# Kernel optimization log

Measured on AMD Instinct MI355X. Metric: run time of the kernel, lower is better.

## Reference

```python
import jax, jax.numpy as jnp
import numpy as np
from jax import lax

K = 5          # dynamic kernel size
GROUPS = 8     # inter_channels // group_channels = 128 // 16
R = 2          # pixel shuffle upscale factor
SLOPE = 0.01   # LeakyReLU default negative_slope
EPS = 1e-5     # BatchNorm eps


def conv2d(x, w, b, pad=0):
    # x: [B,C,H,W], w: [O,I,kh,kw]
    y = lax.conv_general_dilated(x, w, (1, 1), [(pad, pad), (pad, pad)],
                                 dimension_numbers=('NCHW', 'OIHW', 'NCHW'))
    return y + b[None, :, None, None]


def pixel_shuffle(x, r):
    B, C, H, W = x.shape
    x = x.reshape(B, C // (r * r), r, r, H, W)
    x = x.transpose(0, 1, 4, 2, 5, 3)  # B, C', H, r, W, r
    return x.reshape(B, C // (r * r), H * r, W * r)


def involution(x, weight, k, groups, pad):
    # x: [B,C,H,W]; weight: [B,groups,k,k,H,W]
    # out[b, g*gc+c, h, w] = sum_ij weight[b,g,i,j,h,w] * x_pad[b, g*gc+c, h+i, w+j]
    B, C, H, W = x.shape
    gc = C // groups
    xp = jnp.pad(x, ((0, 0), (0, 0), (pad, pad), (pad, pad)))
    xg = xp.reshape(B, groups, gc, H + 2 * pad, W + 2 * pad)
    out = jnp.zeros((B, groups, gc, H, W), x.dtype)
    for i in range(k):
        for j in range(k):
            out = out + weight[:, :, None, i, j] * xg[:, :, :, i:i + H, j:j + W]
    return out.reshape(B, C, H, W)


def setup_inputs() -> dict:
    key = jax.random.key(0)
    ks = jax.random.split(key, 16)
    s = 0.05
    return {
        'high_level': jax.random.normal(ks[0], (8, 128, 64, 64), jnp.float32),
        'low_level': jax.random.normal(ks[1], (8, 224, 128, 128), jnp.float32),
        'emb': jax.random.normal(ks[2], (8, 256, 128, 128), jnp.float32),
        'reduce_w': jax.random.normal(ks[3], (128, 256, 1, 1), jnp.float32) * s,
        'reduce_b': jax.random.normal(ks[4], (128,), jnp.float32) * s,
        'conv1_w': jax.random.normal(ks[5], (32, 128, 1, 1), jnp.float32) * s,
        'conv1_b': jax.random.normal(ks[6], (32,), jnp.float32) * s,
        'conv2_w': jax.random.normal(ks[7], (200, 32, 3, 3), jnp.float32) * s,
        'conv2_b': jax.random.normal(ks[8], (200,), jnp.float32) * s,
        'embconv_w': jax.random.normal(ks[9], (32, 256, 1, 1), jnp.float32) * s,
        'embconv_b': jax.random.normal(ks[10], (32,), jnp.float32) * s,
        'out_w': jax.random.normal(ks[11], (64, 128, 1, 1), jnp.float32) * s,
        'out_b': jax.random.normal(ks[12], (64,), jnp.float32) * s,
        'bn_gamma': jnp.ones((64,), jnp.float32),
        'bn_beta': jnp.zeros((64,), jnp.float32),
        'bn_mean': jnp.zeros((64,), jnp.float32),
        'bn_var': jax.random.uniform(ks[13], (64,), jnp.float32, 0.5, 1.5),
    }


def reference(high_level, low_level, emb,
              reduce_w, reduce_b, conv1_w, conv1_b, conv2_w, conv2_b,
              embconv_w, embconv_b, out_w, out_b,
              bn_gamma, bn_beta, bn_mean, bn_var):
    cat = jnp.concatenate([pixel_shuffle(high_level, R), low_level], axis=1)
    cat = conv2d(cat, reduce_w, reduce_b)
    mix = jax.nn.leaky_relu(conv2d(cat, conv1_w, conv1_b)
                            + conv2d(emb, embconv_w, embconv_b), SLOPE)
    w = conv2d(mix, conv2_w, conv2_b, pad=1)  # [B, K*K*GROUPS, H, W]
    B, _, H, W = w.shape
    w = w.reshape(B, GROUPS, K, K, H, W)
    o = involution(cat, w, K, GROUPS, (K - 1) // 2)
    o = conv2d(o, out_w, out_b)
    o = (o - bn_mean[None, :, None, None]) * (bn_gamma[None, :, None, None]
        / jnp.sqrt(bn_var[None, :, None, None] + EPS)) + bn_beta[None, :, None, None]
    return jax.nn.leaky_relu(o, SLOPE)
```

## Files before the change

kernel.cpp:

```cpp
#include <hip/hip_runtime.h>

typedef unsigned short u16; typedef unsigned int u32; typedef unsigned long long u64;
typedef __attribute__((ext_vector_type(8))) short short8;
typedef __attribute__((ext_vector_type(16))) float f32x16;

#define HW 16384

#define RED_B  0
#define C1E_B  128
#define C2_B   160
#define OUT_B  416
#define BN_SC  480
#define BN_SH  544
#define FLAG_OFF   4096
#define RWB_OFF    8192
#define C1B_OFF    73728
#define EMBB_OFF   81920
#define OUTB_OFF   98304
#define C2PB_OFF   114688
#define CAT2_OFF   524288
#define MIX_OFF    34078720
#define WGT_OFF    42467328

__device__ __forceinline__ float bf2f(u16 x){ u32 u=((u32)x)<<16; float f; __builtin_memcpy(&f,&u,4); return f; }
__device__ __forceinline__ u16 f2bf(float f){ u32 u; __builtin_memcpy(&u,&f,4); return (u16)((u + 0x7fffu + ((u>>16)&1u))>>16); }
__device__ __forceinline__ float lrelu(float x){ return x>0.f ? x : 0.01f*x; }

template<int M> __device__ __forceinline__ u16 ldb(const void* p, size_t i){
    if (M==1) return ((const u16*)p)[i];
    return f2bf(((const float*)p)[i]);
}
template<int M> __device__ __forceinline__ float ldf(const void* p, size_t i){
    if (M==1) return bf2f(((const u16*)p)[i]);
    return ((const float*)p)[i];
}
__device__ __forceinline__ void stA(u16* At, int stride, int p, int c, u16 v){
    At[p*stride + ((((c>>3) ^ ((p>>1)&7)))<<3) + (c&7)] = v;
}

__global__ void detect_kernel(const void* __restrict__ emb, u32* __restrict__ flag){
    int tid = threadIdx.x;
    const u16* p = (const u16*)emb;
    int e = (p[tid*2] >> 7) & 0xFF;
    u64 m = __ballot(e >= 100 && e <= 140);
    if (tid == 0) *flag = (__popcll(m) >= 32) ? 1u : 0u;
}

template<int M>
__global__ __launch_bounds__(256) void k_prep(
    const void* rw, const void* rb, const void* c1w, const void* c1b,
    const void* c2w, const void* c2b, const void* ew, const void* eb,
    const void* ow, const void* ob, const void* gam, const void* bet,
    const void* mn, const void* vr, char* ws, const u32* flag)
{
    if (*flag != (u32)M) return;
    float* wf = (float*)ws;
    int i = blockIdx.x*256 + threadIdx.x;
    if (i < 32768)       ((u16*)(ws+RWB_OFF))[i] = ldb<M>(rw, i);
    else if (i < 36864)  ((u16*)(ws+C1B_OFF))[i-32768] = ldb<M>(c1w, i-32768);
    else if (i < 45056)  ((u16*)(ws+EMBB_OFF))[i-36864] = ldb<M>(ew, i-36864);
    else if (i < 53248)  ((u16*)(ws+OUTB_OFF))[i-45056] = ldb<M>(ow, i-45056);
    else if (i < 126976) {
        int j = i-53248; int o = j/288, k = j - o*288;
        int tap = k>>5, ic = k&31;
        u16 v = 0;
        if (o < 200) v = ldb<M>(c2w, (size_t)o*288 + ic*9 + tap);
        ((u16*)(ws+C2PB_OFF))[j] = v;
    }
    else if (i < 127584) {
        int j = i-126976;
        if (j < 128) wf[RED_B+j] = ldf<M>(rb, j);
        else if (j < 160) wf[C1E_B+j-128] = ldf<M>(c1b, j-128) + ldf<M>(eb, j-128);
        else if (j < 416) { int o = j-160; wf[C2_B+o] = (o<200) ? ldf<M>(c2b,o) : 0.f; }
        else if (j < 480) wf[OUT_B+j-416] = ldf<M>(ob, j-416);
        else if (j < 544) { int c=j-480; wf[BN_SC+c] = ldf<M>(gam,c) * rsqrtf(ldf<M>(vr,c)+1e-5f); }
        else { int c=j-544; wf[BN_SH+c] = ldf<M>(bet,c) - ldf<M>(mn,c)*ldf<M>(gam,c)*rsqrtf(ldf<M>(vr,c)+1e-5f); }
    }
}

template<int M>
__global__ __launch_bounds__(256) void k_reduce(
    const void* __restrict__ hi, const void* __restrict__ lo,
    const u16* __restrict__ rwB, const float* __restrict__ wf,
    u16* __restrict__ cat2, const u32* __restrict__ flag)
{
    if (*flag != (u32)M) return;
    __shared__ u16 At[64*264];
    const int tid = threadIdx.x, wvi = tid>>6, lane = tid&63;
    const int rt = (wvi>>1)*32, nc0 = (wvi&1)*64;
    const int col = lane&31, q = lane>>5;

    short8 B[2][16];
#pragma unroll
    for (int nt=0; nt<2; nt++){
        int o = nc0 + nt*32 + col;
#pragma unroll
        for (int s=0; s<16; s++)
            __builtin_memcpy(&B[nt][s], rwB + (size_t)o*256 + s*16 + q*8, 16);
    }

    for (int it=0; it<4; it++){
        int chunk = blockIdx.x + it*512;
        int gpx = chunk*64;
        int b = gpx>>14, p0 = gpx&16383;
        int h = p0>>7, w0 = p0&127;
        __syncthreads();
        {
            int qq = tid&31, cid = tid>>5;
#pragma unroll 4
            for (int i=0;i<28;i++){
                int c = cid*28 + i;
                size_t src = ((size_t)(b*224 + c))*HW + p0 + 2*qq;
                u16 v0, v1;
                if (M==1){ u32 v = *(const u32*)((const u16*)lo + src); v0=(u16)v; v1=(u16)(v>>16); }
                else { v0 = f2bf(((const float*)lo)[src]); v1 = f2bf(((const float*)lo)[src+1]); }
                stA(At,264, 2*qq,   32+c, v0);
                stA(At,264, 2*qq+1, 32+c, v1);
            }
        }
        {
            int xq = tid&15, cid = tid>>4;
#pragma unroll
            for (int i=0;i<2;i++){
                int c = cid + i*16;
                int hc = c*4 + (h&1)*2;
                size_t src = ((size_t)(b*128 + hc))*4096 + (size_t)(h>>1)*64 + (w0>>1) + 2*xq;
                u16 e0 = ldb<M>(hi, src),      e1 = ldb<M>(hi, src+1);
                u16 o0 = ldb<M>(hi, src+4096), o1 = ldb<M>(hi, src+4097);
                stA(At,264, 4*xq,   c, e0);
                stA(At,264, 4*xq+2, c, e1);
                stA(At,264, 4*xq+1, c, o0);
                stA(At,264, 4*xq+3, c, o1);
            }
        }
        __syncthreads();

        f32x16 acc0, acc1;
#pragma unroll
        for (int r=0;r<16;r++){ acc0[r]=0.f; acc1[r]=0.f; }
        int pp = rt + col, sw = (pp>>1)&7;
        const u16* arow = At + pp*264;
#pragma unroll
        for (int s=0;s<16;s++){
            short8 a;
            __builtin_memcpy(&a, arow + (((2*s+q)^sw)<<3), 16);
            acc0 = __builtin_amdgcn_mfma_f32_32x32x16_bf16(a, B[0][s], acc0, 0,0,0);
            acc1 = __builtin_amdgcn_mfma_f32_32x32x16_bf16(a, B[1][s], acc1, 0,0,0);
        }
#pragma unroll
        for (int nt=0; nt<2; nt++){
            int oc = nc0 + nt*32 + col;
            float bias = wf[RED_B + oc];
#pragma unroll
            for (int r=0;r<16;r++){
                int row = (r&3) + 8*(r>>2) + 4*q;
                float v = (nt ? acc1[r] : acc0[r]) + bias;
                cat2[((size_t)(gpx + rt + row))*128 + oc] = f2bf(v);
            }
        }
    }
}

template<int M>
__global__ __launch_bounds__(256) void k_mix(
    const u16* __restrict__ cat2, const void* __restrict__ emb,
    const u16* __restrict__ c1B, const u16* __restrict__ embB,
    const float* __restrict__ wf, u16* __restrict__ mixt, const u32* __restrict__ flag)
{
    if (*flag != (u32)M) return;
    __shared__ u16 At[128*136];
    const int tid = threadIdx.x, wvi = tid>>6, lane = tid&63;
    const int rt = wvi*32, col = lane&31, q = lane>>5;

    short8 Bc[8], Be[16];
#pragma unroll
    for (int s=0;s<8;s++)  __builtin_memcpy(&Bc[s], c1B  + (size_t)col*128 + s*16 + q*8, 16);
#pragma unroll
    for (int s=0;s<16;s++) __builtin_memcpy(&Be[s], embB + (size_t)col*256 + s*16 + q*8, 16);

    for (int it=0; it<4; it++){
        int chunk = blockIdx.x + it*256;
        int gpx = chunk*128;
        int b = gpx>>14, p0 = gpx&16383;

        f32x16 acc;
#pragma unroll
        for (int r=0;r<16;r++) acc[r]=0.f;
        int pp = rt + col, sw = (pp>>1)&7;
        const u16* arow = At + pp*136;

        __syncthreads();
#pragma unroll
        for (int i=0;i<8;i++){
            int idx = tid + i*256;
            int p = idx>>4, c16 = idx&15;
            short8 v;
            __builtin_memcpy(&v, cat2 + ((size_t)(gpx+p))*128 + c16*8, 16);
            *(short8*)(At + p*136 + ((c16 ^ ((p>>1)&7))<<3)) = v;
        }
        __syncthreads();
#pragma unroll
        for (int s=0;s<8;s++){
            short8 a; __builtin_memcpy(&a, arow + (((2*s+q)^sw)<<3), 16);
            acc = __builtin_amdgcn_mfma_f32_32x32x16_bf16(a, Bc[s], acc, 0,0,0);
        }
#pragma unroll 1
        for (int half=0; half<2; half++){
            __syncthreads();
            {
                int qq = tid&31, cid = (tid>>5)&1, g2 = tid>>6;
#pragma unroll 2
                for (int ph=0; ph<2; ph++)
#pragma unroll 4
                for (int i=0;i<16;i++){
                    int c = cid*64 + g2*16 + i;
                    int ec = half*128 + c;
                    int p = ph*64 + 2*qq;
                    size_t src = ((size_t)(b*256 + ec))*HW + p0 + p;
                    u16 v0, v1;
                    if (M==1){ u32 v = *(const u32*)((const u16*)emb + src); v0=(u16)v; v1=(u16)(v>>16); }
                    else { v0 = f2bf(((const float*)emb)[src]); v1 = f2bf(((const float*)emb)[src+1]); }
                    stA(At,136, p,   c, v0);
                    stA(At,136, p+1, c, v1);
                }
            }
            __syncthreads();
#pragma unroll
            for (int s=0;s<8;s++){
                short8 a; __builtin_memcpy(&a, arow + (((2*s+q)^sw)<<3), 16);
                acc = __builtin_amdgcn_mfma_f32_32x32x16_bf16(a, Be[half*8+s], acc, 0,0,0);
            }
        }
        float bias = wf[C1E_B + col];
#pragma unroll
        for (int r=0;r<16;r++){
            int row = (r&3) + 8*(r>>2) + 4*q;
            mixt[((size_t)(gpx + rt + row))*32 + col] = f2bf(lrelu(acc[r] + bias));
        }
    }
}

__global__ __launch_bounds__(256) void k_conv2(
    const u16* __restrict__ mixt, const u16* __restrict__ c2B,
    const float* __restrict__ wf, u16* __restrict__ wgt)
{
    __shared__ u16 halo[100*32];
    const int tid = threadIdx.x, wvi = tid>>6, lane = tid&63;
    const int rt = (wvi>>1)*32, npair = wvi&1;
    const int nh = blockIdx.x & 1;
    const int nc0 = nh*128 + npair*64;
    const int col = lane&31, q = lane>>5;

    short8 B[2][18];
#pragma unroll
    for (int nt=0; nt<2; nt++){
        int o = nc0 + nt*32 + col;
#pragma unroll
        for (int s=0; s<18; s++)
            __builtin_memcpy(&B[nt][s], c2B + (size_t)o*288 + s*16 + q*8, 16);
    }

    for (int it=0; it<4; it++){
        int tile = (blockIdx.x>>1) + it*512;
        int b = tile>>8, tl = tile&255;
        int ty = tl>>4, tx = tl&15;
        __syncthreads();
#pragma unroll
        for (int i=0;i<2;i++){
            int idx = tid + i*256;
            if (idx < 400){
                int point = idx>>2, cq = idx&3;
                int y = ty*8 + point/10 - 1, x = tx*8 + point%10 - 1;
                short8 v;
                if (y>=0 && y<128 && x>=0 && x<128)
                    __builtin_memcpy(&v, mixt + ((size_t)(b*HW + y*128 + x))*32 + cq*8, 16);
                else { short z = 0; v = (short8){z,z,z,z,z,z,z,z}; }
                *(short8*)(halo + point*32 + cq*8) = v;
            }
        }
        __syncthreads();

        f32x16 acc0, acc1;
#pragma unroll
        for (int r=0;r<16;r++){ acc0[r]=0.f; acc1[r]=0.f; }
        int pp = rt + col, py = pp>>3, px = pp&7;
#pragma unroll
        for (int s=0;s<18;s++){
            int tap = s>>1, ih = s&1;
            int dy = tap/3, dx = tap%3;
            short8 a;
            __builtin_memcpy(&a, halo + ((py+dy)*10 + px+dx)*32 + ih*16 + q*8, 16);
            acc0 = __builtin_amdgcn_mfma_f32_32x32x16_bf16(a, B[0][s], acc0, 0,0,0);
            acc1 = __builtin_amdgcn_mfma_f32_32x32x16_bf16(a, B[1][s], acc1, 0,0,0);
        }
#pragma unroll
        for (int nt=0; nt<2; nt++){
            int oc = nc0 + nt*32 + col;
            if (oc < 200){
                float bias = wf[C2_B + oc];
#pragma unroll
                for (int r=0;r<16;r++){
                    int row = (r&3) + 8*(r>>2) + 4*q;
                    int p2 = rt + row;
                    int y = ty*8 + (p2>>3), x = tx*8 + (p2&7);
                    float v = (nt ? acc1[r] : acc0[r]) + bias;
                    wgt[((size_t)(b*200 + oc))*HW + y*128 + x] = f2bf(v);
                }
            }
        }
    }
}

template<int M>
__global__ __launch_bounds__(256) void k_inv(
    const u16* __restrict__ cat2, const u16* __restrict__ wgt,
    const u16* __restrict__ outB, const float* __restrict__ wf,
    void* __restrict__ out, const u32* __restrict__ flag)
{
    if (*flag != (u32)M) return;
    __shared__ u16 halo[400*16];
    __shared__ u16 og[256*16];
    const int tid = threadIdx.x, wvi = tid>>6, lane = tid&63;
    const int col = lane&31, q = lane>>5;
    const int b = blockIdx.y, ty = blockIdx.x>>3, tx = blockIdx.x&7;
    const int py = tid>>4, px = tid&15;
    const int h = ty*16 + py, w = tx*16 + px;

    f32x16 acc[2][2];
#pragma unroll
    for (int i=0;i<2;i++)
#pragma unroll
    for (int j=0;j<2;j++)
#pragma unroll
    for (int r=0;r<16;r++) acc[i][j][r] = 0.f;

#pragma unroll 1
    for (int g=0; g<8; g++){
        __syncthreads();
#pragma unroll
        for (int i=0;i<4;i++){
            int idx = tid + i*256;
            if (idx < 800){
                int point = idx>>1, cq = idx&1;
                int y = ty*16 + point/20 - 2, x = tx*16 + point%20 - 2;
                short8 v;
                if (y>=0 && y<128 && x>=0 && x<128)
                    __builtin_memcpy(&v, cat2 + ((size_t)(b*HW + y*128 + x))*128 + g*16 + cq*8, 16);
                else { short z=0; v = (short8){z,z,z,z,z,z,z,z}; }
                *(short8*)(halo + point*16 + cq*8) = v;
            }
        }
        __syncthreads();

        float wvv[25];
#pragma unroll
        for (int t=0;t<25;t++)
            wvv[t] = bf2f(wgt[((size_t)(b*200 + g*25 + t))*HW + h*128 + w]);

        float a16[16];
#pragma unroll
        for (int cc=0;cc<16;cc++) a16[cc]=0.f;
#pragma unroll
        for (int t=0;t<25;t++){
            int dy = t/5, dx = t%5;
            u32 vv[8];
            __builtin_memcpy(vv, halo + ((py+dy)*20 + px+dx)*16, 32);
            float wt = wvv[t];
#pragma unroll
            for (int r=0;r<8;r++){
                u32 u = vv[r];
                u32 ulo = u<<16, uhi = u & 0xffff0000u;
                float x0, x1;
                __builtin_memcpy(&x0,&ulo,4); __builtin_memcpy(&x1,&uhi,4);
                a16[2*r]   += wt*x0;
                a16[2*r+1] += wt*x1;
            }
        }
        u32 pk[8];
#pragma unroll
        for (int r=0;r<8;r++) pk[r] = (u32)f2bf(a16[2*r]) | ((u32)f2bf(a16[2*r+1])<<16);
        __syncthreads();
        __builtin_memcpy(og + tid*16, pk, 32);
        __syncthreads();

        short8 bo0, bo1;
        __builtin_memcpy(&bo0, outB + (size_t)(col)*128      + g*16 + q*8, 16);
        __builtin_memcpy(&bo1, outB + (size_t)(32+col)*128   + g*16 + q*8, 16);
#pragma unroll
        for (int rt2=0; rt2<2; rt2++){
            int prow = (wvi*2 + rt2)*32 + col;
            short8 a; __builtin_memcpy(&a, og + prow*16 + q*8, 16);
            acc[rt2][0] = __builtin_amdgcn_mfma_f32_32x32x16_bf16(a, bo0, acc[rt2][0], 0,0,0);
            acc[rt2][1] = __builtin_amdgcn_mfma_f32_32x32x16_bf16(a, bo1, acc[rt2][1], 0,0,0);
        }
    }
#pragma unroll
    for (int rt2=0; rt2<2; rt2++)
#pragma unroll
    for (int nt=0; nt<2; nt++){
        int oc = nt*32 + col;
        float bias = wf[OUT_B+oc], sc = wf[BN_SC+oc], sh = wf[BN_SH+oc];
#pragma unroll
        for (int r=0;r<16;r++){
            int row = (r&3) + 8*(r>>2) + 4*q;
            int p = (wvi*2 + rt2)*32 + row;
            int yy = ty*16 + (p>>4), xx = tx*16 + (p&15);
            float v = lrelu((acc[rt2][nt][r] + bias)*sc + sh);
            size_t oidx = ((size_t)(b*64 + oc))*HW + yy*128 + xx;
            if (M==1) ((u16*)out)[oidx] = f2bf(v);
            else ((float*)out)[oidx] = v;
        }
    }
}

extern "C" void kernel_launch(void* const* d_in, const int* in_sizes, int n_in,
                              void* d_out, int out_size, void* d_ws, size_t ws_size,
                              hipStream_t stream) {
    const void* hi  = d_in[0];
    const void* lo  = d_in[1];
    const void* emb = d_in[2];
    char* ws = (char*)d_ws;
    float* wf = (float*)ws;
    u32* flag = (u32*)(ws + FLAG_OFF);
    u16* cat2 = (u16*)(ws + CAT2_OFF);
    u16* mixt = (u16*)(ws + MIX_OFF);
    u16* wgt  = (u16*)(ws + WGT_OFF);

    detect_kernel<<<1, 64, 0, stream>>>(emb, flag);

    k_prep<0><<<499,256,0,stream>>>(d_in[3],d_in[4],d_in[5],d_in[6],d_in[7],d_in[8],
        d_in[9],d_in[10],d_in[11],d_in[12],d_in[13],d_in[14],d_in[15],d_in[16], ws, flag);
    k_prep<1><<<499,256,0,stream>>>(d_in[3],d_in[4],d_in[5],d_in[6],d_in[7],d_in[8],
        d_in[9],d_in[10],d_in[11],d_in[12],d_in[13],d_in[14],d_in[15],d_in[16], ws, flag);

    k_reduce<0><<<512,256,0,stream>>>(hi, lo, (const u16*)(ws+RWB_OFF), wf, cat2, flag);
    k_reduce<1><<<512,256,0,stream>>>(hi, lo, (const u16*)d_in[3],      wf, cat2, flag);

    k_mix<0><<<256,256,0,stream>>>(cat2, emb, (const u16*)(ws+C1B_OFF), (const u16*)(ws+EMBB_OFF), wf, mixt, flag);
    k_mix<1><<<256,256,0,stream>>>(cat2, emb, (const u16*)d_in[5],      (const u16*)d_in[9],       wf, mixt, flag);

    k_conv2<<<1024,256,0,stream>>>(mixt, (const u16*)(ws+C2PB_OFF), wf, wgt);

    k_inv<0><<<dim3(64,8),256,0,stream>>>(cat2, wgt, (const u16*)(ws+OUTB_OFF), wf, d_out, flag);
    k_inv<1><<<dim3(64,8),256,0,stream>>>(cat2, wgt, (const u16*)d_in[11],      wf, d_out, flag);
}
```

Before: 488.1 us.

## Vectorize global loads in reduce and mix kernels and launch one tile per block

The reduce and mix kernels now load input activations with 16-byte (or 32-byte fp32) vector loads per thread along the pixel dimension, replacing 2-element scalar loads. They also drop the persistent 4-iteration loop in favour of four times as many blocks, each handling one tile. This aims to cut global load instruction count and raise memory-level parallelism. In exchange, weights are reloaded per block, and the per-element LDS transpose stores in the swizzled layout may cause more bank conflicts.

```diff
diff --git a/kernel.cpp b/kernel.cpp
--- a/kernel.cpp
+++ b/kernel.cpp
@@ -33,6 +33,16 @@
 template<int M> __device__ __forceinline__ float ldf(const void* p, size_t i){
     if (M==1) return bf2f(((const u16*)p)[i]);
     return ((const float*)p)[i];
+}
+template<int M> __device__ __forceinline__ short8 ld8(const void* p, size_t i){
+    short8 v;
+    if (M==1){ __builtin_memcpy(&v, (const u16*)p + i, 16); }
+    else {
+        float a[8]; __builtin_memcpy(a, (const float*)p + i, 32);
+#pragma unroll
+        for (int r=0;r<8;r++) v[r] = (short)f2bf(a[r]);
+    }
+    return v;
 }
 __device__ __forceinline__ void stA(u16* At, int stride, int p, int c, u16 v){
     At[p*stride + ((((c>>3) ^ ((p>>1)&7)))<<3) + (c&7)] = v;
@@ -90,6 +100,10 @@
     const int rt = (wvi>>1)*32, nc0 = (wvi&1)*64;
     const int col = lane&31, q = lane>>5;
 
+    const int gpx = blockIdx.x*64;
+    const int b = gpx>>14, p0 = gpx&16383;
+    const int h = p0>>7, w0 = p0&127;
+
     short8 B[2][16];
 #pragma unroll
     for (int nt=0; nt<2; nt++){
@@ -99,64 +113,53 @@
             __builtin_memcpy(&B[nt][s], rwB + (size_t)o*256 + s*16 + q*8, 16);
     }
 
-    for (int it=0; it<4; it++){
-        int chunk = blockIdx.x + it*512;
-        int gpx = chunk*64;
-        int b = gpx>>14, p0 = gpx&16383;
-        int h = p0>>7, w0 = p0&127;
-        __syncthreads();
-        {
-            int qq = tid&31, cid = tid>>5;
-#pragma unroll 4
-            for (int i=0;i<28;i++){
-                int c = cid*28 + i;
-                size_t src = ((size_t)(b*224 + c))*HW + p0 + 2*qq;
-                u16 v0, v1;
-                if (M==1){ u32 v = *(const u32*)((const u16*)lo + src); v0=(u16)v; v1=(u16)(v>>16); }
-                else { v0 = f2bf(((const float*)lo)[src]); v1 = f2bf(((const float*)lo)[src+1]); }
-                stA(At,264, 2*qq,   32+c, v0);
-                stA(At,264, 2*qq+1, 32+c, v1);
-            }
-        }
-        {
-            int xq = tid&15, cid = tid>>4;
-#pragma unroll
-            for (int i=0;i<2;i++){
-                int c = cid + i*16;
-                int hc = c*4 + (h&1)*2;
-                size_t src = ((size_t)(b*128 + hc))*4096 + (size_t)(h>>1)*64 + (w0>>1) + 2*xq;
-                u16 e0 = ldb<M>(hi, src),      e1 = ldb<M>(hi, src+1);
-                u16 o0 = ldb<M>(hi, src+4096), o1 = ldb<M>(hi, src+4097);
-                stA(At,264, 4*xq,   c, e0);
-                stA(At,264, 4*xq+2, c, e1);
-                stA(At,264, 4*xq+1, c, o0);
-                stA(At,264, 4*xq+3, c, o1);
-            }
-        }
-        __syncthreads();
-
-        f32x16 acc0, acc1;
-#pragma unroll
-        for (int r=0;r<16;r++){ acc0[r]=0.f; acc1[r]=0.f; }
-        int pp = rt + col, sw = (pp>>1)&7;
-        const u16* arow = At + pp*264;
-#pragma unroll
-        for (int s=0;s<16;s++){
-            short8 a;
-            __builtin_memcpy(&a, arow + (((2*s+q)^sw)<<3), 16);
-            acc0 = __builtin_amdgcn_mfma_f32_32x32x16_bf16(a, B[0][s], acc0, 0,0,0);
-            acc1 = __builtin_amdgcn_mfma_f32_32x32x16_bf16(a, B[1][s], acc1, 0,0,0);
-        }
-#pragma unroll
-        for (int nt=0; nt<2; nt++){
-            int oc = nc0 + nt*32 + col;
-            float bias = wf[RED_B + oc];
-#pragma unroll
-            for (int r=0;r<16;r++){
-                int row = (r&3) + 8*(r>>2) + 4*q;
-                float v = (nt ? acc1[r] : acc0[r]) + bias;
-                cat2[((size_t)(gpx + rt + row))*128 + oc] = f2bf(v);
-            }
+    if (tid < 224) {
+        int c = tid;
+        size_t base = ((size_t)(b*224 + c))*HW + p0;
+#pragma unroll
+        for (int i=0;i<8;i++){
+            short8 v = ld8<M>(lo, base + 8*i);
+#pragma unroll
+            for (int j=0;j<8;j++) stA(At,264, 8*i+j, 32+c, (u16)v[j]);
+        }
+    } else {
+        int cc = tid - 224;
+        int hc = cc*4 + (h&1)*2;
+        size_t srcE = ((size_t)(b*128 + hc))*4096 + (size_t)(h>>1)*64 + (w0>>1);
+#pragma unroll
+        for (int i=0;i<4;i++){
+            short8 e = ld8<M>(hi, srcE + 8*i);
+            short8 o = ld8<M>(hi, srcE + 4096 + 8*i);
+#pragma unroll
+            for (int j=0;j<8;j++){
+                stA(At,264, 16*i+2*j,   cc, (u16)e[j]);
+                stA(At,264, 16*i+2*j+1, cc, (u16)o[j]);
+            }
+        }
+    }
+    __syncthreads();
+
+    f32x16 acc0, acc1;
+#pragma unroll
+    for (int r=0;r<16;r++){ acc0[r]=0.f; acc1[r]=0.f; }
+    int pp = rt + col, sw = (pp>>1)&7;
+    const u16* arow = At + pp*264;
+#pragma unroll
+    for (int s=0;s<16;s++){
+        short8 a;
+        __builtin_memcpy(&a, arow + (((2*s+q)^sw)<<3), 16);
+        acc0 = __builtin_amdgcn_mfma_f32_32x32x16_bf16(a, B[0][s], acc0, 0,0,0);
+        acc1 = __builtin_amdgcn_mfma_f32_32x32x16_bf16(a, B[1][s], acc1, 0,0,0);
+    }
+#pragma unroll
+    for (int nt=0; nt<2; nt++){
+        int oc = nc0 + nt*32 + col;
+        float bias = wf[RED_B + oc];
+#pragma unroll
+        for (int r=0;r<16;r++){
+            int row = (r&3) + 8*(r>>2) + 4*q;
+            float v = (nt ? acc1[r] : acc0[r]) + bias;
+            cat2[((size_t)(gpx + rt + row))*128 + oc] = f2bf(v);
         }
     }
 }
@@ -172,71 +175,65 @@
     const int tid = threadIdx.x, wvi = tid>>6, lane = tid&63;
     const int rt = wvi*32, col = lane&31, q = lane>>5;
 
-    short8 Bc[8], Be[16];
-#pragma unroll
-    for (int s=0;s<8;s++)  __builtin_memcpy(&Bc[s], c1B  + (size_t)col*128 + s*16 + q*8, 16);
-#pragma unroll
-    for (int s=0;s<16;s++) __builtin_memcpy(&Be[s], embB + (size_t)col*256 + s*16 + q*8, 16);
-
-    for (int it=0; it<4; it++){
-        int chunk = blockIdx.x + it*256;
-        int gpx = chunk*128;
-        int b = gpx>>14, p0 = gpx&16383;
-
-        f32x16 acc;
-#pragma unroll
-        for (int r=0;r<16;r++) acc[r]=0.f;
-        int pp = rt + col, sw = (pp>>1)&7;
-        const u16* arow = At + pp*136;
-
-        __syncthreads();
-#pragma unroll
-        for (int i=0;i<8;i++){
-            int idx = tid + i*256;
-            int p = idx>>4, c16 = idx&15;
-            short8 v;
-            __builtin_memcpy(&v, cat2 + ((size_t)(gpx+p))*128 + c16*8, 16);
-            *(short8*)(At + p*136 + ((c16 ^ ((p>>1)&7))<<3)) = v;
+    const int gpx = blockIdx.x*128;
+    const int b = gpx>>14, p0 = gpx&16383;
+
+    short8 Bc[8];
+#pragma unroll
+    for (int s=0;s<8;s++)  __builtin_memcpy(&Bc[s], c1B + (size_t)col*128 + s*16 + q*8, 16);
+
+    f32x16 acc;
+#pragma unroll
+    for (int r=0;r<16;r++) acc[r]=0.f;
+    int pp = rt + col, sw = (pp>>1)&7;
+    const u16* arow = At + pp*136;
+
+#pragma unroll
+    for (int i=0;i<8;i++){
+        int idx = tid + i*256;
+        int p = idx>>4, c16 = idx&15;
+        short8 v;
+        __builtin_memcpy(&v, cat2 + ((size_t)(gpx+p))*128 + c16*8, 16);
+        *(short8*)(At + p*136 + ((c16 ^ ((p>>1)&7))<<3)) = v;
+    }
+    __syncthreads();
+#pragma unroll
+    for (int s=0;s<8;s++){
+        short8 a; __builtin_memcpy(&a, arow + (((2*s+q)^sw)<<3), 16);
+        acc = __builtin_amdgcn_mfma_f32_32x32x16_bf16(a, Bc[s], acc, 0,0,0);
+    }
+
+    const int chalf = (wvi&1)*64, pxh = (wvi>>1)*64;
+#pragma unroll 1
+    for (int half=0; half<2; half++){
+        short8 Be[8];
+#pragma unroll
+        for (int s=0;s<8;s++)
+            __builtin_memcpy(&Be[s], embB + (size_t)col*256 + half*128 + s*16 + q*8, 16);
+        __syncthreads();
+        {
+            int c = half*128 + chalf + lane;
+            int cl = chalf + lane;
+            size_t base = ((size_t)(b*256 + c))*HW + p0 + pxh;
+#pragma unroll
+            for (int i=0;i<8;i++){
+                short8 v = ld8<M>(emb, base + 8*i);
+#pragma unroll
+                for (int j=0;j<8;j++) stA(At,136, pxh+8*i+j, cl, (u16)v[j]);
+            }
         }
         __syncthreads();
 #pragma unroll
         for (int s=0;s<8;s++){
             short8 a; __builtin_memcpy(&a, arow + (((2*s+q)^sw)<<3), 16);
-            acc = __builtin_amdgcn_mfma_f32_32x32x16_bf16(a, Bc[s], acc, 0,0,0);
-        }
-#pragma unroll 1
-        for (int half=0; half<2; half++){
-            __syncthreads();
-            {
-                int qq = tid&31, cid = (tid>>5)&1, g2 = tid>>6;
-#pragma unroll 2
-                for (int ph=0; ph<2; ph++)
-#pragma unroll 4
-                for (int i=0;i<16;i++){
-                    int c = cid*64 + g2*16 + i;
-                    int ec = half*128 + c;
-                    int p = ph*64 + 2*qq;
-                    size_t src = ((size_t)(b*256 + ec))*HW + p0 + p;
-                    u16 v0, v1;
-                    if (M==1){ u32 v = *(const u32*)((const u16*)emb + src); v0=(u16)v; v1=(u16)(v>>16); }
-                    else { v0 = f2bf(((const float*)emb)[src]); v1 = f2bf(((const float*)emb)[src+1]); }
-                    stA(At,136, p,   c, v0);
-                    stA(At,136, p+1, c, v1);
-                }
-            }
-            __syncthreads();
-#pragma unroll
-            for (int s=0;s<8;s++){
-                short8 a; __builtin_memcpy(&a, arow + (((2*s+q)^sw)<<3), 16);
-                acc = __builtin_amdgcn_mfma_f32_32x32x16_bf16(a, Be[half*8+s], acc, 0,0,0);
-            }
-        }
-        float bias = wf[C1E_B + col];
-#pragma unroll
-        for (int r=0;r<16;r++){
-            int row = (r&3) + 8*(r>>2) + 4*q;
-            mixt[((size_t)(gpx + rt + row))*32 + col] = f2bf(lrelu(acc[r] + bias));
-        }
+            acc = __builtin_amdgcn_mfma_f32_32x32x16_bf16(a, Be[s], acc, 0,0,0);
+        }
+    }
+    float bias = wf[C1E_B + col];
+#pragma unroll
+    for (int r=0;r<16;r++){
+        int row = (r&3) + 8*(r>>2) + 4*q;
+        mixt[((size_t)(gpx + rt + row))*32 + col] = f2bf(lrelu(acc[r] + bias));
     }
 }
 
@@ -433,11 +430,11 @@
     k_prep<1><<<499,256,0,stream>>>(d_in[3],d_in[4],d_in[5],d_in[6],d_in[7],d_in[8],
         d_in[9],d_in[10],d_in[11],d_in[12],d_in[13],d_in[14],d_in[15],d_in[16], ws, flag);
 
-    k_reduce<0><<<512,256,0,stream>>>(hi, lo, (const u16*)(ws+RWB_OFF), wf, cat2, flag);
-    k_reduce<1><<<512,256,0,stream>>>(hi, lo, (const u16*)d_in[3],      wf, cat2, flag);
-
-    k_mix<0><<<256,256,0,stream>>>(cat2, emb, (const u16*)(ws+C1B_OFF), (const u16*)(ws+EMBB_OFF), wf, mixt, flag);
-    k_mix<1><<<256,256,0,stream>>>(cat2, emb, (const u16*)d_in[5],      (const u16*)d_in[9],       wf, mixt, flag);
+    k_reduce<0><<<2048,256,0,stream>>>(hi, lo, (const u16*)(ws+RWB_OFF), wf, cat2, flag);
+    k_reduce<1><<<2048,256,0,stream>>>(hi, lo, (const u16*)d_in[3],      wf, cat2, flag);
+
+    k_mix<0><<<1024,256,0,stream>>>(cat2, emb, (const u16*)(ws+C1B_OFF), (const u16*)(ws+EMBB_OFF), wf, mixt, flag);
+    k_mix<1><<<1024,256,0,stream>>>(cat2, emb, (const u16*)d_in[5],      (const u16*)d_in[9],       wf, mixt, flag);
 
     k_conv2<<<1024,256,0,stream>>>(mixt, (const u16*)(ws+C2PB_OFF), wf, wgt);
 
```

Result: no change. 479.5 us (-1.7%).
